# Optimization experiments

Measured on AMD Instinct MI355X. Metric: run time of the kernel, lower is better.

## Reference

```python
import jax, jax.numpy as jnp
import numpy as np

BATCH, T, FEAT, HID = 64, 8192, 512, 256


def setup_inputs() -> dict:
    key = jax.random.key(0)
    kA, kB, kW, kb = jax.random.split(key, 4)
    A = jax.random.normal(kA, (BATCH, FEAT), dtype=jnp.float32)
    B = jax.random.normal(kB, (BATCH, T, HID), dtype=jnp.float32)
    # torch.nn.Linear(feature_dim, hidden_dim): weight [hid, feat], bias [hid]
    W = jax.random.normal(kW, (HID, FEAT), dtype=jnp.float32) * (1.0 / np.sqrt(FEAT))
    b = jax.random.normal(kb, (HID,), dtype=jnp.float32) * 0.01
    return {"A": A, "B": B, "W": W, "b": b}


def reference(A, B, W, b):
    # query projection: [batch, hid]
    AP = jnp.tanh(A @ W.T + b)
    # scores: query (len 1) against all T timesteps -> [batch, T]
    R = jnp.einsum('bh,bth->bt', AP, B)
    R = jnp.exp(-R)
    R = R / jnp.sum(R, axis=-1, keepdims=True)
    # attention pooling over time: [batch, hid]
    Con = jnp.einsum('bt,bth->bh', R, B)
    # original returns [batch, 1, hid] (squeeze(2) is a no-op for hid>1)
    return Con[:, None, :]
```

## Files before the change

kernel.cpp:

```cpp
#include <hip/hip_runtime.h>


#define BATCH 64
#define T_LEN 8192
#define FEAT 512
#define HID 256
#define SPLIT 32
#define ROWS_PER_BLOCK (T_LEN / SPLIT)
#define ROWS_PER_WAVE 64
#define ITERS (ROWS_PER_WAVE / 8)

typedef float f4 __attribute__((ext_vector_type(4)));

__device__ __forceinline__ f4 ntl(const f4* p) { return __builtin_nontemporal_load(p); }
__device__ __forceinline__ float hsum(f4 v) { return (v.x + v.y) + (v.z + v.w); }

__global__ __launch_bounds__(256) void ap_kernel(const float* __restrict__ A,
                                                 const float* __restrict__ W,
                                                 const float* __restrict__ bias,
                                                 float* __restrict__ AP) {
    const int b = blockIdx.x;
    const int tid = threadIdx.x;

    __shared__ float sA[FEAT];
    __shared__ float sW[HID * 33];

    sA[tid] = A[b * FEAT + tid];
    sA[tid + 256] = A[b * FEAT + tid + 256];

    float acc = 0.0f;
    for (int k0 = 0; k0 < FEAT; k0 += 32) {
        __syncthreads();
        #pragma unroll
        for (int t = 0; t < 8; ++t) {
            int f = t * 256 + tid;
            int h = f >> 3;
            int kq = f & 7;
            float4 v = *(const float4*)(W + (size_t)h * FEAT + k0 + kq * 4);
            float* dst = &sW[h * 33 + kq * 4];
            dst[0] = v.x; dst[1] = v.y; dst[2] = v.z; dst[3] = v.w;
        }
        __syncthreads();
        #pragma unroll
        for (int k = 0; k < 32; ++k)
            acc += sA[k0 + k] * sW[tid * 33 + k];
    }
    acc += bias[tid];
    AP[b * HID + tid] = tanhf(acc);
}

__global__ __launch_bounds__(256) void pool_kernel(const float* __restrict__ B,
                                                   const float* __restrict__ AP,
                                                   float* __restrict__ numP,
                                                   float* __restrict__ denP) {
    const int split = blockIdx.x;
    const int b = blockIdx.y;
    const int tid = threadIdx.x;
    const int wv = tid >> 6;
    const int lane = tid & 63;
    const int sub = lane >> 4;
    const int pos = lane & 15;

    const f4* __restrict__ AP4 = (const f4*)(AP + b * HID);
    const f4 ap0 = AP4[pos];
    const f4 ap1 = AP4[pos + 16];
    const f4 ap2 = AP4[pos + 32];
    const f4 ap3 = AP4[pos + 48];

    const f4* __restrict__ B4 = (const f4*)(B) + (size_t)b * T_LEN * (HID / 4);
    const int row0 = split * ROWS_PER_BLOCK + wv * ROWS_PER_WAVE;

    f4 acc0 = {0.f,0.f,0.f,0.f}, acc1 = {0.f,0.f,0.f,0.f};
    f4 acc2 = {0.f,0.f,0.f,0.f}, acc3 = {0.f,0.f,0.f,0.f};
    float den = 0.0f;

    const f4* pa = B4 + (size_t)(row0 + sub) * (HID / 4);
    const f4* pb = pa + 4 * (HID / 4);
    f4 vA0 = ntl(pa + pos), vA1 = ntl(pa + pos + 16), vA2 = ntl(pa + pos + 32), vA3 = ntl(pa + pos + 48);
    f4 vB0 = ntl(pb + pos), vB1 = ntl(pb + pos + 16), vB2 = ntl(pb + pos + 32), vB3 = ntl(pb + pos + 48);

    #pragma unroll
    for (int it = 0; it < ITERS; ++it) {
        const int nit = (it + 1 < ITERS) ? it + 1 : ITERS - 1;
        const f4* na = B4 + (size_t)(row0 + nit * 8 + sub) * (HID / 4);
        const f4* nb = na + 4 * (HID / 4);
        f4 nA0 = ntl(na + pos), nA1 = ntl(na + pos + 16), nA2 = ntl(na + pos + 32), nA3 = ntl(na + pos + 48);
        f4 nB0 = ntl(nb + pos), nB1 = ntl(nb + pos + 16), nB2 = ntl(nb + pos + 32), nB3 = ntl(nb + pos + 48);

        f4 mA = vA0 * ap0 + vA1 * ap1 + vA2 * ap2 + vA3 * ap3;
        f4 mB = vB0 * ap0 + vB1 * ap1 + vB2 * ap2 + vB3 * ap3;
        float pAs = hsum(mA);
        float pBs = hsum(mB);

        pAs += __shfl_xor(pAs, 8, 64);
        pBs += __shfl_xor(pBs, 8, 64);
        pAs += __shfl_xor(pAs, 4, 64);
        pBs += __shfl_xor(pBs, 4, 64);
        pAs += __shfl_xor(pAs, 2, 64);
        pBs += __shfl_xor(pBs, 2, 64);
        pAs += __shfl_xor(pAs, 1, 64);
        pBs += __shfl_xor(pBs, 1, 64);

        const float wA = __expf(-pAs);
        const float wB = __expf(-pBs);
        acc0 += wA * vA0 + wB * vB0;
        acc1 += wA * vA1 + wB * vB1;
        acc2 += wA * vA2 + wB * vB2;
        acc3 += wA * vA3 + wB * vB3;
        den += wA + wB;

        vA0 = nA0; vA1 = nA1; vA2 = nA2; vA3 = nA3;
        vB0 = nB0; vB1 = nB1; vB2 = nB2; vB3 = nB3;
    }

    #define XRED(x) x += __shfl_xor(x, 16, 64); x += __shfl_xor(x, 32, 64)
    XRED(acc0.x); XRED(acc0.y); XRED(acc0.z); XRED(acc0.w);
    XRED(acc1.x); XRED(acc1.y); XRED(acc1.z); XRED(acc1.w);
    XRED(acc2.x); XRED(acc2.y); XRED(acc2.z); XRED(acc2.w);
    XRED(acc3.x); XRED(acc3.y); XRED(acc3.z); XRED(acc3.w);
    XRED(den);
    #undef XRED

    __shared__ float s_num[4][HID];
    __shared__ float s_den[4];
    if (sub == 0) {
        f4* dst = (f4*)s_num[wv];
        dst[pos]      = acc0;
        dst[pos + 16] = acc1;
        dst[pos + 32] = acc2;
        dst[pos + 48] = acc3;
    }
    if (lane == 0) s_den[wv] = den;
    __syncthreads();

    const int blk = b * SPLIT + split;
    float n = s_num[0][tid] + s_num[1][tid] + s_num[2][tid] + s_num[3][tid];
    numP[(size_t)blk * HID + tid] = n;
    if (tid == 0) denP[blk] = s_den[0] + s_den[1] + s_den[2] + s_den[3];
}

__global__ __launch_bounds__(256) void reduce_kernel(const float* __restrict__ numP,
                                                     const float* __restrict__ denP,
                                                     float* __restrict__ out) {
    const int b = blockIdx.x;
    const int h = threadIdx.x;
    float num = 0.0f, den = 0.0f;
    #pragma unroll
    for (int s = 0; s < SPLIT; ++s) {
        num += numP[(size_t)(b * SPLIT + s) * HID + h];
        den += denP[b * SPLIT + s];
    }
    out[b * HID + h] = num / den;
}

extern "C" void kernel_launch(void* const* d_in, const int* in_sizes, int n_in,
                              void* d_out, int out_size, void* d_ws, size_t ws_size,
                              hipStream_t stream) {
    const float* A = (const float*)d_in[0];
    const float* B = (const float*)d_in[1];
    const float* W = (const float*)d_in[2];
    const float* bias = (const float*)d_in[3];
    float* out = (float*)d_out;

    float* AP = (float*)d_ws;
    float* numP = AP + BATCH * HID;
    float* denP = numP + BATCH * SPLIT * HID;

    ap_kernel<<<BATCH, 256, 0, stream>>>(A, W, bias, AP);
    pool_kernel<<<dim3(SPLIT, BATCH), 256, 0, stream>>>(B, AP, numP, denP);
    reduce_kernel<<<BATCH, 256, 0, stream>>>(numP, denP, out);
}
```

Before: 107.5 us.

## Split projection across more blocks, use DPP reductions, drop redundant tail prefetch

The projection kernel now runs on a 4x64 grid: each block handles 64 hidden units, with 16 lanes per row doing vectorized dot products reduced by DPP row operations, replacing the shared-memory tiled loop on only 64 blocks. In the pooling kernel, the shuffle-based 16-lane reduction is replaced by DPP adds. The redundant reload on the final iteration is also skipped. The intent is to raise parallelism in the small projection stage and cut cross-lane and memory overhead, at the cost of reading W directly from global memory in every block.

After: 96.48 us (median of 2 runs). 1.11x faster.

```diff
diff --git a/kernel.cpp b/kernel.cpp
--- a/kernel.cpp
+++ b/kernel.cpp
@@ -15,38 +15,46 @@
 __device__ __forceinline__ f4 ntl(const f4* p) { return __builtin_nontemporal_load(p); }
 __device__ __forceinline__ float hsum(f4 v) { return (v.x + v.y) + (v.z + v.w); }
 
+template <int CTRL>
+__device__ __forceinline__ float dpp_add(float x) {
+    int y = __builtin_amdgcn_update_dpp(0, __float_as_int(x), CTRL, 0xF, 0xF, true);
+    return x + __int_as_float(y);
+}
+__device__ __forceinline__ float row16_allreduce(float x) {
+    x = dpp_add<0xB1>(x);
+    x = dpp_add<0x4E>(x);
+    x = dpp_add<0x128>(x);
+    x = dpp_add<0x124>(x);
+    return x;
+}
+
 __global__ __launch_bounds__(256) void ap_kernel(const float* __restrict__ A,
                                                  const float* __restrict__ W,
                                                  const float* __restrict__ bias,
                                                  float* __restrict__ AP) {
-    const int b = blockIdx.x;
+    const int p = blockIdx.x;
+    const int b = blockIdx.y;
     const int tid = threadIdx.x;
+    const int pos = tid & 15;
 
     __shared__ float sA[FEAT];
-    __shared__ float sW[HID * 33];
-
     sA[tid] = A[b * FEAT + tid];
     sA[tid + 256] = A[b * FEAT + tid + 256];
+    __syncthreads();
 
-    float acc = 0.0f;
-    for (int k0 = 0; k0 < FEAT; k0 += 32) {
-        __syncthreads();
-        #pragma unroll
-        for (int t = 0; t < 8; ++t) {
-            int f = t * 256 + tid;
-            int h = f >> 3;
-            int kq = f & 7;
-            float4 v = *(const float4*)(W + (size_t)h * FEAT + k0 + kq * 4);
-            float* dst = &sW[h * 33 + kq * 4];
-            dst[0] = v.x; dst[1] = v.y; dst[2] = v.z; dst[3] = v.w;
-        }
-        __syncthreads();
-        #pragma unroll
-        for (int k = 0; k < 32; ++k)
-            acc += sA[k0 + k] * sW[tid * 33 + k];
+    const f4* sA4 = (const f4*)sA;
+    f4 a0 = sA4[pos],      a1 = sA4[pos + 16], a2 = sA4[pos + 32], a3 = sA4[pos + 48];
+    f4 a4 = sA4[pos + 64], a5 = sA4[pos + 80], a6 = sA4[pos + 96], a7 = sA4[pos + 112];
+
+    #pragma unroll
+    for (int pass = 0; pass < 4; ++pass) {
+        const int h = p * 64 + pass * 16 + (tid >> 4);
+        const f4* Wr = (const f4*)(W + (size_t)h * FEAT);
+        f4 m = Wr[pos] * a0 + Wr[pos + 16] * a1 + Wr[pos + 32] * a2 + Wr[pos + 48] * a3
+             + Wr[pos + 64] * a4 + Wr[pos + 80] * a5 + Wr[pos + 96] * a6 + Wr[pos + 112] * a7;
+        float s = row16_allreduce(hsum(m));
+        if (pos == 0) AP[b * HID + h] = tanhf(s + bias[h]);
     }
-    acc += bias[tid];
-    AP[b * HID + tid] = tanhf(acc);
 }
 
 __global__ __launch_bounds__(256) void pool_kernel(const float* __restrict__ B,
@@ -81,25 +89,23 @@
 
     #pragma unroll
     for (int it = 0; it < ITERS; ++it) {
-        const int nit = (it + 1 < ITERS) ? it + 1 : ITERS - 1;
-        const f4* na = B4 + (size_t)(row0 + nit * 8 + sub) * (HID / 4);
-        const f4* nb = na + 4 * (HID / 4);
-        f4 nA0 = ntl(na + pos), nA1 = ntl(na + pos + 16), nA2 = ntl(na + pos + 32), nA3 = ntl(na + pos + 48);
-        f4 nB0 = ntl(nb + pos), nB1 = ntl(nb + pos + 16), nB2 = ntl(nb + pos + 32), nB3 = ntl(nb + pos + 48);
+        f4 nA0, nA1, nA2, nA3, nB0, nB1, nB2, nB3;
+        if (it + 1 < ITERS) {
+            const f4* na = B4 + (size_t)(row0 + (it + 1) * 8 + sub) * (HID / 4);
+            const f4* nb = na + 4 * (HID / 4);
+            nA0 = ntl(na + pos); nA1 = ntl(na + pos + 16); nA2 = ntl(na + pos + 32); nA3 = ntl(na + pos + 48);
+            nB0 = ntl(nb + pos); nB1 = ntl(nb + pos + 16); nB2 = ntl(nb + pos + 32); nB3 = ntl(nb + pos + 48);
+        }
 
         f4 mA = vA0 * ap0 + vA1 * ap1 + vA2 * ap2 + vA3 * ap3;
         f4 mB = vB0 * ap0 + vB1 * ap1 + vB2 * ap2 + vB3 * ap3;
         float pAs = hsum(mA);
         float pBs = hsum(mB);
 
-        pAs += __shfl_xor(pAs, 8, 64);
-        pBs += __shfl_xor(pBs, 8, 64);
-        pAs += __shfl_xor(pAs, 4, 64);
-        pBs += __shfl_xor(pBs, 4, 64);
-        pAs += __shfl_xor(pAs, 2, 64);
-        pBs += __shfl_xor(pBs, 2, 64);
-        pAs += __shfl_xor(pAs, 1, 64);
-        pBs += __shfl_xor(pBs, 1, 64);
+        pAs = dpp_add<0xB1>(pAs);  pBs = dpp_add<0xB1>(pBs);
+        pAs = dpp_add<0x4E>(pAs);  pBs = dpp_add<0x4E>(pBs);
+        pAs = dpp_add<0x128>(pAs); pBs = dpp_add<0x128>(pBs);
+        pAs = dpp_add<0x124>(pAs); pBs = dpp_add<0x124>(pBs);
 
         const float wA = __expf(-pAs);
         const float wB = __expf(-pBs);
@@ -109,8 +115,10 @@
         acc3 += wA * vA3 + wB * vB3;
         den += wA + wB;
 
-        vA0 = nA0; vA1 = nA1; vA2 = nA2; vA3 = nA3;
-        vB0 = nB0; vB1 = nB1; vB2 = nB2; vB3 = nB3;
+        if (it + 1 < ITERS) {
+            vA0 = nA0; vA1 = nA1; vA2 = nA2; vA3 = nA3;
+            vB0 = nB0; vB1 = nB1; vB2 = nB2; vB3 = nB3;
+        }
     }
 
     #define XRED(x) x += __shfl_xor(x, 16, 64); x += __shfl_xor(x, 32, 64)
@@ -166,7 +174,7 @@
     float* numP = AP + BATCH * HID;
     float* denP = numP + BATCH * SPLIT * HID;
 
-    ap_kernel<<<BATCH, 256, 0, stream>>>(A, W, bias, AP);
+    ap_kernel<<<dim3(4, BATCH), 256, 0, stream>>>(A, W, bias, AP);
     pool_kernel<<<dim3(SPLIT, BATCH), 256, 0, stream>>>(B, AP, numP, denP);
     reduce_kernel<<<BATCH, 256, 0, stream>>>(numP, denP, out);
 }
```
